# Kernel optimization log

Measured on AMD Instinct MI355X. Metric: run time of the kernel, lower is better.

## Reference

```python
import jax, jax.numpy as jnp
import numpy as np
from functools import partial

MIN_PERSISTENCE = 0.0
BIG = jnp.float32(1e30)


def pairwise_dist(points):
    # points: [n, d] -> [n, n] Euclidean distances (Vietoris-Rips filtration values on edges)
    sq = jnp.sum(points * points, axis=-1)
    d2 = sq[:, None] + sq[None, :] - 2.0 * (points @ points.T)
    return jnp.sqrt(jnp.clip(d2, 0.0))


def h0_persistence(points):
    """0-dim persistent homology of the Vietoris-Rips filtration.

    H0 bars: every point is born at filtration 0; components merge at MST edge
    lengths (single-linkage). Deaths = the n-1 MST edge weights, in the order
    Prim's algorithm adds them (the boundary-matrix column reduction for dim 0
    yields exactly these pairs). One essential class (infinite bar) is dropped.
    """
    n = points.shape[0]
    dist = pairwise_dist(points)  # [n, n]

    in_tree = jnp.zeros((n,), dtype=bool).at[0].set(True)
    mind = dist[0]  # min distance from each node to the current tree

    def step(carry, _):
        mind, in_tree = carry
        masked = jnp.where(in_tree, BIG, mind)
        j = jnp.argmin(masked)          # next vertex merged into the tree
        death = masked[j]               # filtration value at which its component dies
        in_tree = in_tree.at[j].set(True)
        mind = jnp.minimum(mind, dist[j])
        return (mind, in_tree), death

    (_, _), deaths = jax.lax.scan(step, (mind, in_tree), None, length=n - 1)

    births = jnp.zeros_like(deaths)
    diagram = jnp.stack([births, deaths], axis=-1)  # [n-1, 2]
    # min_persistence threshold: zero out bars with persistence below threshold
    keep = (deaths - births) >= MIN_PERSISTENCE
    return jnp.where(keep[:, None], diagram, 0.0)


def setup_inputs() -> dict:
    key = jax.random.key(0)
    x = jax.random.normal(key, (8192, 64), dtype=jnp.float32)
    return {"x": x}


def reference(x):
    # PersistentHomologyLayer.forward with edge_index=None -> point-cloud VR persistence.
    return h0_persistence(x)
```

## Files before the change

kernel.cpp:

```cpp
#include <hip/hip_runtime.h>
#include <math.h>

#define N 8192
#define DIM 64
#define CAP_E 2000000

typedef unsigned long long u64;
typedef unsigned int u32;
typedef unsigned short u16;

__global__ void zero_out_kernel(float* __restrict__ out, int n) {
    int i = blockIdx.x * blockDim.x + threadIdx.x;
    if (i < n) out[i] = 0.0f;
}

__global__ __launch_bounds__(256) void norms_kernel(const float* __restrict__ x,
                                                    float* __restrict__ norms) {
    int i = blockIdx.x * blockDim.x + threadIdx.x;
    const float* row = x + (size_t)i * DIM;
    float acc = 0.f;
    #pragma unroll
    for (int k = 0; k < DIM; k++) { float v = row[k]; acc = __builtin_fmaf(v, v, acc); }
    norms[i] = acc;
}

__device__ inline void stage_tiles(const float* __restrict__ x, int bi, int bj, int t,
                                   float (*As)[64], float (*Bs)[64]) {
    int r = t >> 2, c0 = (t & 3) * 16;
    const float4* pa = (const float4*)(x + (size_t)(bi * 64 + r) * DIM + c0);
    const float4* pb = (const float4*)(x + (size_t)(bj * 64 + r) * DIM + c0);
    #pragma unroll
    for (int q = 0; q < 4; q++) {
        float4 a = pa[q], b = pb[q];
        int c = c0 + q * 4;
        As[c + 0][r] = a.x; As[c + 1][r] = a.y; As[c + 2][r] = a.z; As[c + 3][r] = a.w;
        Bs[c + 0][r] = b.x; Bs[c + 1][r] = b.y; Bs[c + 2][r] = b.z; Bs[c + 3][r] = b.w;
    }
}

__device__ inline void tile_d2(const float (*As)[64], const float (*Bs)[64],
                               const float ni[4], const float nj[4],
                               int tx, int ty, u32 d2b[4][4]) {
    float acc[4][4] = {};
    #pragma unroll 4
    for (int k = 0; k < 64; k++) {
        float av[4], bv[4];
        #pragma unroll
        for (int r = 0; r < 4; r++) av[r] = As[k][ty * 4 + r];
        #pragma unroll
        for (int c = 0; c < 4; c++) bv[c] = Bs[k][tx * 4 + c];
        #pragma unroll
        for (int r = 0; r < 4; r++)
            #pragma unroll
            for (int c = 0; c < 4; c++)
                acc[r][c] = __builtin_fmaf(av[r], bv[c], acc[r][c]);
    }
    #pragma unroll
    for (int r = 0; r < 4; r++)
        #pragma unroll
        for (int c = 0; c < 4; c++) {
            float d2 = __builtin_fmaf(-2.0f, acc[r][c], ni[r] + nj[c]);
            d2 = d2 < 0.f ? 0.f : d2;
            d2b[r][c] = __float_as_uint(d2);
        }
}

__global__ void init_kernel(u64* bestR, u64* bestC, u16* comp16, u32* deg, u32* ctr) {
    int i = blockIdx.x * blockDim.x + threadIdx.x;
    if (i < 8192) { bestR[i] = ~0ull; bestC[i] = ~0ull; comp16[i] = (u16)i; deg[i] = 0; }
    if (i < 8) ctr[i] = 0;
}

__global__ __launch_bounds__(256) void scan_fused(const float* __restrict__ x,
                                                  const float* __restrict__ norms,
                                                  const u16* __restrict__ comp16,
                                                  u64* __restrict__ bestR,
                                                  const u32* __restrict__ ctr) {
    if (ctr[1]) return;
    int bi = blockIdx.y, bj = blockIdx.x;
    if (bj < bi) return;
    __shared__ float As[64][64], Bs[64][64];
    __shared__ u16 rc[64], cc[64];
    __shared__ u64 rowBest[64], colBest[64];
    int t = threadIdx.x;
    stage_tiles(x, bi, bj, t, As, Bs);
    if (t < 64) {
        rc[t] = comp16[bi * 64 + t];
        cc[t] = comp16[bj * 64 + t];
        rowBest[t] = ~0ull; colBest[t] = ~0ull;
    }
    __syncthreads();
    int tx = t & 15, ty = t >> 4;
    float ni[4], nj[4];
    #pragma unroll
    for (int r = 0; r < 4; r++) ni[r] = norms[bi * 64 + ty * 4 + r];
    #pragma unroll
    for (int c = 0; c < 4; c++) nj[c] = norms[bj * 64 + tx * 4 + c];
    u32 d2b[4][4];
    tile_d2(As, Bs, ni, nj, tx, ty, d2b);

    #pragma unroll
    for (int r = 0; r < 4; r++) {
        u16 rcv = rc[ty * 4 + r];
        int gi = bi * 64 + ty * 4 + r;
        u64 best = ~0ull;
        #pragma unroll
        for (int c = 0; c < 4; c++) {
            if (cc[tx * 4 + c] != rcv) {
                int gj = bj * 64 + tx * 4 + c;
                u32 lo = gi < gj ? (u32)gi : (u32)gj;
                u32 hi = gi < gj ? (u32)gj : (u32)gi;
                u64 key = ((u64)d2b[r][c] << 26) | ((u64)lo << 13) | hi;
                if (key < best) best = key;
            }
        }
        if (best != ~0ull) atomicMin(&rowBest[ty * 4 + r], best);
    }
    #pragma unroll
    for (int c = 0; c < 4; c++) {
        u16 ccv = cc[tx * 4 + c];
        int gj = bj * 64 + tx * 4 + c;
        u64 best = ~0ull;
        #pragma unroll
        for (int r = 0; r < 4; r++) {
            if (rc[ty * 4 + r] != ccv) {
                int gi = bi * 64 + ty * 4 + r;
                u32 lo = gi < gj ? (u32)gi : (u32)gj;
                u32 hi = gi < gj ? (u32)gj : (u32)gi;
                u64 key = ((u64)d2b[r][c] << 26) | ((u64)lo << 13) | hi;
                if (key < best) best = key;
            }
        }
        if (best != ~0ull) atomicMin(&colBest[tx * 4 + c], best);
    }
    __syncthreads();
    if (t < 64) {
        if (rowBest[t] != ~0ull) atomicMin(&bestR[bi * 64 + t], rowBest[t]);
        if (colBest[t] != ~0ull) atomicMin(&bestR[bj * 64 + t], colBest[t]);
    }
}

__global__ void fold_kernel(u64* bestR, u64* bestC, const u16* comp16, const u32* ctr) {
    if (ctr[1]) return;
    int i = blockIdx.x * blockDim.x + threadIdx.x;
    if (i < 8192) {
        u64 k = bestR[i];
        if (k != ~0ull) { atomicMin(&bestC[comp16[i]], k); bestR[i] = ~0ull; }
    }
}

__global__ __launch_bounds__(1024) void merge_kernel(u16* comp16, u64* bestC,
                                                     u64* mstKeys, u32* ctr) {
    __shared__ u16 ping[8192], pong[8192];
    __shared__ unsigned char act[8192];
    __shared__ u32 cnt_s;
    if (ctr[1]) return;
    int t = threadIdx.x;
    if (t == 0) cnt_s = 0;
    for (int c = t; c < 8192; c += 1024) {
        u64 key = bestC[c];
        u16 par = (u16)c;
        if (key != ~0ull) {
            u32 a = (u32)(key >> 13) & 8191u, b = (u32)key & 8191u;
            u16 ca = comp16[a];
            u16 cv = (ca == (u16)c) ? comp16[b] : ca;
            u64 k2 = bestC[cv];
            bool mutual = false;
            if (k2 != ~0ull) {
                u32 a2 = (u32)(k2 >> 13) & 8191u, b2 = (u32)k2 & 8191u;
                u16 ca2 = comp16[a2];
                u16 cv2 = (ca2 == cv) ? comp16[b2] : ca2;
                mutual = (cv2 == (u16)c);
            }
            par = cv;
            if (mutual && (u32)c < (u32)cv) par = (u16)c;
            bool add = (!mutual) || ((u32)c < (u32)cv);
            if (add) {
                u32 idx = atomicAdd(&ctr[0], 1u);
                if (idx < 8192u) mstKeys[idx] = key;
            }
        }
        ping[c] = par;
        act[c] = 0;
    }
    __syncthreads();
    for (int c = t; c < 8192; c += 1024) bestC[c] = ~0ull;
    __syncthreads();
    for (int it = 0; it < 13; it++) {
        for (int c = t; c < 8192; c += 1024) pong[c] = ping[ping[c]];
        __syncthreads();
        for (int c = t; c < 8192; c += 1024) ping[c] = pong[c];
        __syncthreads();
    }
    for (int v = t; v < 8192; v += 1024) {
        u16 nc = ping[comp16[v]];
        comp16[v] = nc;
        act[nc] = 1;
    }
    __syncthreads();
    u32 local = 0;
    for (int c = t; c < 8192; c += 1024) local += act[c];
    atomicAdd(&cnt_s, local);
    __syncthreads();
    if (t == 0 && cnt_s == 1) ctr[1] = 1;
}

__global__ __launch_bounds__(1024) void sort_kernel(const u64* __restrict__ mstKeys,
                                                    u32* __restrict__ sortedWB,
                                                    const u32* __restrict__ ctr) {
    __shared__ u64 keys[8192];
    int t = threadIdx.x;
    u32 m = ctr[0]; if (m > 8191u) m = 8191u;
    for (int i = t; i < 8192; i += 1024) keys[i] = (i < (int)m) ? mstKeys[i] : ~0ull;
    __syncthreads();
    for (u32 k = 2; k <= 8192; k <<= 1)
        for (u32 j = k >> 1; j > 0; j >>= 1) {
            for (int i = t; i < 8192; i += 1024) {
                u32 ixj = (u32)i ^ j;
                if (ixj > (u32)i) {
                    u64 a = keys[i], b = keys[ixj];
                    bool up = ((i & k) == 0);
                    if ((a > b) == up) { keys[i] = b; keys[ixj] = a; }
                }
            }
            __syncthreads();
        }
    for (int i = t; i < 8192; i += 1024)
        sortedWB[i] = (i < 8191) ? (u32)(keys[i] >> 26) : 0xFFFFFFFFu;
}

__global__ __launch_bounds__(256) void collect_kernel(const float* __restrict__ x,
                                                      const float* __restrict__ norms,
                                                      const u32* __restrict__ sortedWB,
                                                      u64* __restrict__ edges,
                                                      u32* __restrict__ ctr) {
    __shared__ float As[64][64], Bs[64][64];
    __shared__ u32 sw[8191];
    int bi = blockIdx.y, bj = blockIdx.x;
    if (bj < bi) return;
    int t = threadIdx.x;
    stage_tiles(x, bi, bj, t, As, Bs);
    for (int i = t; i < 8191; i += 256) sw[i] = sortedWB[i];
    __syncthreads();
    u32 wmin = sw[0], wmax = sw[8190];
    int tx = t & 15, ty = t >> 4;
    float ni[4], nj[4];
    #pragma unroll
    for (int r = 0; r < 4; r++) ni[r] = norms[bi * 64 + ty * 4 + r];
    #pragma unroll
    for (int c = 0; c < 4; c++) nj[c] = norms[bj * 64 + tx * 4 + c];
    u32 d2b[4][4];
    tile_d2(As, Bs, ni, nj, tx, ty, d2b);

    #pragma unroll
    for (int r = 0; r < 4; r++) {
        int gi = bi * 64 + ty * 4 + r;
        #pragma unroll
        for (int c = 0; c < 4; c++) {
            int gj = bj * 64 + tx * 4 + c;
            if (gj <= gi) continue;
            u32 wb = d2b[r][c];
            if (wb < wmin || wb > wmax) continue;
            int lo = 0, hi = 8190;
            while (lo < hi) { int mid = (lo + hi) >> 1; if (sw[mid] < wb) lo = mid + 1; else hi = mid; }
            if (sw[lo] == wb) {
                u32 idx = atomicAdd(&ctr[3], 1u);
                if (idx < CAP_E)
                    edges[idx] = ((u64)(u32)lo << 26) | ((u64)(u32)gi << 13) | (u32)gj;
                else
                    atomicOr(&ctr[2], 16u);
            }
        }
    }
}

__global__ void degcnt_kernel(const u64* __restrict__ edges, u32* __restrict__ deg,
                              const u32* __restrict__ ctr) {
    u32 m = ctr[3]; if (m > CAP_E) m = CAP_E;
    for (u32 idx = blockIdx.x * 256u + threadIdx.x; idx < m; idx += gridDim.x * 256u) {
        u64 e = edges[idx];
        atomicAdd(&deg[(u32)(e >> 13) & 8191u], 1u);
        atomicAdd(&deg[(u32)e & 8191u], 1u);
    }
}

__global__ __launch_bounds__(1024) void offs_kernel(const u32* __restrict__ deg,
                                                    u32* __restrict__ offs,
                                                    u32* __restrict__ cur) {
    __shared__ u32 partial[1024];
    int t = threadIdx.x;
    u32 loc[8], s = 0;
    #pragma unroll
    for (int e = 0; e < 8; e++) { loc[e] = deg[t * 8 + e]; s += loc[e]; }
    partial[t] = s;
    __syncthreads();
    for (int d = 1; d < 1024; d <<= 1) {
        u32 v = (t >= d) ? partial[t - d] : 0;
        __syncthreads();
        partial[t] += v;
        __syncthreads();
    }
    u32 run = t ? partial[t - 1] : 0;
    #pragma unroll
    for (int e = 0; e < 8; e++) { offs[t * 8 + e] = run; cur[t * 8 + e] = run; run += loc[e]; }
    if (t == 1023) offs[8192] = run;
}

__global__ void fill_kernel(const u64* __restrict__ edges, u32* __restrict__ cur,
                            u32* __restrict__ adj, const u32* __restrict__ ctr) {
    u32 m = ctr[3]; if (m > CAP_E) m = CAP_E;
    for (u32 idx = blockIdx.x * 256u + threadIdx.x; idx < m; idx += gridDim.x * 256u) {
        u64 e = edges[idx];
        u32 rk = (u32)(e >> 26) & 8191u;
        u32 i = (u32)(e >> 13) & 8191u, j = (u32)e & 8191u;
        u32 p1 = atomicAdd(&cur[i], 1u); adj[p1] = (rk << 13) | j;
        u32 p2 = atomicAdd(&cur[j], 1u); adj[p2] = (rk << 13) | i;
    }
}

__device__ __forceinline__ u32 dpp_min_u32(u32 x) {
    u32 y;
    y = (u32)__builtin_amdgcn_update_dpp((int)0xFFFFFFFF, (int)x, 0x111, 0xf, 0xf, false); x = y < x ? y : x;
    y = (u32)__builtin_amdgcn_update_dpp((int)0xFFFFFFFF, (int)x, 0x112, 0xf, 0xf, false); x = y < x ? y : x;
    y = (u32)__builtin_amdgcn_update_dpp((int)0xFFFFFFFF, (int)x, 0x114, 0xf, 0xf, false); x = y < x ? y : x;
    y = (u32)__builtin_amdgcn_update_dpp((int)0xFFFFFFFF, (int)x, 0x118, 0xf, 0xf, false); x = y < x ? y : x;
    y = (u32)__builtin_amdgcn_update_dpp((int)0xFFFFFFFF, (int)x, 0x142, 0xa, 0xf, false); x = y < x ? y : x;
    y = (u32)__builtin_amdgcn_update_dpp((int)0xFFFFFFFF, (int)x, 0x143, 0xc, 0xf, false); x = y < x ? y : x;
    return x;
}

__global__ __launch_bounds__(256) void gprim_kernel(const u32* __restrict__ offs,
                                                    const u32* __restrict__ adjG,
                                                    u32* __restrict__ seqv,
                                                    u32* __restrict__ ctr) {
    __shared__ u16 sMind[8192];
    __shared__ u32 sOffs[8193];
    __shared__ u32 sAdj[16384];
    const int t = threadIdx.x;
    for (int i = t; i < 8193; i += 256) sOffs[i] = offs[i];
    { u32* p = (u32*)sMind; for (int i = t; i < 4096; i += 256) p[i] = 0x3FFF3FFFu; }
    u32 m = ctr[3]; if (m > CAP_E) m = CAP_E;
    u32 tot = 2u * m;
    const bool useLds = (tot <= 16384u);
    if (useLds) {
        const uint4* a4 = (const uint4*)adjG; uint4* s4 = (uint4*)sAdj;
        u32 tot4 = (tot + 3u) >> 2;
        for (u32 i = (u32)t; i < tot4; i += 256u) s4[i] = a4[i];
    }
    __syncthreads();
    if (t >= 64) return;
    const int lane = t;
    if (lane == 0) sMind[0] = 0xFFFFu;
    u64 ins0 = (lane == 0) ? 1ull : 0ull, ins1 = 0ull;
    u32 cmin = 0xFFFFFFFFu;
    u32 v = 0u, Lv = 0u;

#define PROC(e, pred) do { \
        u32 _far = (e) & 8191u, _rk = (e) >> 13; \
        if ((pred) && (((_far ^ (u32)lane) & 63u) == 0u)) { \
            u32 _slot = _far >> 6; \
            u64 _w = (_slot & 64u) ? ins1 : ins0; \
            if (((_w >> (_slot & 63u)) & 1ull) == 0ull) { \
                u32 _k = (_rk << 13) | _far; \
                if (_k < patch) patch = _k; \
                u32 _loc = ((u32)lane << 7) + _slot; \
                u16 _old = sMind[_loc]; \
                if ((u16)_rk < _old) sMind[_loc] = (u16)_rk; \
            } \
        } \
    } while (0)

    for (int step = 0; step < N - 1; ++step) {
        u32 rowPair = ((const u32*)sMind)[(Lv << 6) + (u32)lane];
        u32 o0 = sOffs[v], o1 = sOffs[v + 1];
        u32 dg = o1 - o0;
        u32 iL = (o1 > o0) ? (o1 - 1u) : o0;
        u32 patch = 0xFFFFFFFFu;
        {
            u32 i1 = (o0 + 1u > iL) ? iL : o0 + 1u;
            u32 i2 = (o0 + 2u > iL) ? iL : o0 + 2u;
            u32 i3 = (o0 + 3u > iL) ? iL : o0 + 3u;
            u32 e0, e1, e2, e3;
            if (useLds) { e0 = sAdj[o0]; e1 = sAdj[i1]; e2 = sAdj[i2]; e3 = sAdj[i3]; }
            else        { e0 = adjG[o0]; e1 = adjG[i1]; e2 = adjG[i2]; e3 = adjG[i3]; }
            PROC(e0, dg > 0u); PROC(e1, dg > 1u); PROC(e2, dg > 2u); PROC(e3, dg > 3u);
            for (u32 q = 4u; q < dg; ++q) {
                u32 e = useLds ? sAdj[o0 + q] : adjG[o0 + q];
                PROC(e, true);
            }
        }
        cmin = patch < cmin ? patch : cmin;
        u32 m0 = rowPair & 0xFFFFu, m1 = rowPair >> 16;
        u32 s0 = ((u32)lane << 1), s1 = s0 + 1u;
        u32 vslot = v >> 6;
        u32 k0 = (m0 < 0x3FFFu && s0 != vslot) ? ((m0 << 13) | (s0 << 6) | Lv) : 0xFFFFFFFFu;
        u32 k1 = (m1 < 0x3FFFu && s1 != vslot) ? ((m1 << 13) | (s1 << 6) | Lv) : 0xFFFFFFFFu;
        u32 rowMin = k0 < k1 ? k0 : k1;
        u32 R = dpp_min_u32(rowMin);
        u32 xc = ((u32)lane == Lv) ? patch : cmin;
        u32 C = dpp_min_u32(xc);
        u32 Rs = (u32)__builtin_amdgcn_readlane((int)R, 63);
        u32 Cs = (u32)__builtin_amdgcn_readlane((int)C, 63);
        u32 g = Rs < Cs ? Rs : Cs;
        if ((u32)lane == Lv) cmin = Rs < patch ? Rs : patch;
        if (g >= (0x3FFFu << 13)) { if (lane == 0) atomicOr(&ctr[2], 2u); break; }
        if (lane == 0) seqv[step] = g;
        v = g & 8191u; Lv = v & 63u;
        if ((u32)lane == Lv) {
            u32 nslot = v >> 6;
            if (nslot < 64u) ins0 |= 1ull << nslot; else ins1 |= 1ull << (nslot - 64u);
            sMind[(Lv << 7) + nslot] = 0xFFFFu;
        }
    }
#undef PROC
}

__global__ void gather_kernel(const u32* __restrict__ seqv,
                              const u32* __restrict__ sortedWB,
                              float* __restrict__ out) {
    int s = blockIdx.x * blockDim.x + threadIdx.x;
    if (s < N - 1) {
        u32 p = seqv[s];
        u32 rk = p >> 13;
        out[2 * s + 1] = sqrtf(__uint_as_float(sortedWB[rk]));
    }
}

extern "C" void kernel_launch(void* const* d_in, const int* in_sizes, int n_in,
                              void* d_out, int out_size, void* d_ws, size_t ws_size,
                              hipStream_t stream) {
    const float* x = (const float*)d_in[0];
    float* out = (float*)d_out;

    char* ws = (char*)d_ws;
    size_t o = 0;
    u64* bestR    = (u64*)(ws + o); o += 8192 * 8;
    u64* bestC    = (u64*)(ws + o); o += 8192 * 8;
    u64* mstKeys  = (u64*)(ws + o); o += 8192 * 8;
    u64* edges    = (u64*)(ws + o); o += (size_t)CAP_E * 8;
    float* norms  = (float*)(ws + o); o += 8192 * 4;
    u32* sortedWB = (u32*)(ws + o); o += 8192 * 4;
    u32* deg      = (u32*)(ws + o); o += 8192 * 4;
    u32* offs     = (u32*)(ws + o); o += 8200 * 4;
    u32* cur      = (u32*)(ws + o); o += 8192 * 4;
    u32* seqv     = (u32*)(ws + o); o += 8192 * 4;
    u32* adj      = (u32*)(ws + o); o += (size_t)CAP_E * 2 * 4;
    u16* comp16   = (u16*)(ws + o); o += 8192 * 2;
    u32* ctr      = (u32*)(ws + o); o += 256;

    zero_out_kernel<<<(out_size + 255) / 256, 256, 0, stream>>>(out, out_size);
    norms_kernel<<<32, 256, 0, stream>>>(x, norms);
    init_kernel<<<32, 256, 0, stream>>>(bestR, bestC, comp16, deg, ctr);

    for (int r = 0; r < 13; r++) {
        scan_fused<<<dim3(128, 128), 256, 0, stream>>>(x, norms, comp16, bestR, ctr);
        fold_kernel<<<32, 256, 0, stream>>>(bestR, bestC, comp16, ctr);
        merge_kernel<<<1, 1024, 0, stream>>>(comp16, bestC, mstKeys, ctr);
    }

    sort_kernel<<<1, 1024, 0, stream>>>(mstKeys, sortedWB, ctr);
    collect_kernel<<<dim3(128, 128), 256, 0, stream>>>(x, norms, sortedWB, edges, ctr);
    degcnt_kernel<<<512, 256, 0, stream>>>(edges, deg, ctr);
    offs_kernel<<<1, 1024, 0, stream>>>(deg, offs, cur);
    fill_kernel<<<512, 256, 0, stream>>>(edges, cur, adj, ctr);
    gprim_kernel<<<1, 256, 0, stream>>>(offs, adj, seqv, ctr);
    gather_kernel<<<32, 256, 0, stream>>>(seqv, sortedWB, out);
}
```

Baseline: 7.181 ms.

## Pack per-vertex adjacency into LDS uint4 slots and pad GEMM tiles

Adds a kernel that packs the first three or four neighbours of each vertex into a 16-byte slot, plus an overflow record for high-degree vertices. The single-block Prim kernel then does one LDS load per step instead of offset lookups and clamped indexing, and falls back to global memory only for vertices with more than four neighbours. It also pads the shared tile arrays to 65 columns to avoid LDS bank conflicts in the distance tiles. The overflow path now always reads global memory even when the full adjacency would have fit in LDS, and the extra kernel adds a launch.

```diff
diff --git a/kernel.cpp b/kernel.cpp
--- a/kernel.cpp
+++ b/kernel.cpp
@@ -25,7 +25,7 @@
 }
 
 __device__ inline void stage_tiles(const float* __restrict__ x, int bi, int bj, int t,
-                                   float (*As)[64], float (*Bs)[64]) {
+                                   float (*As)[65], float (*Bs)[65]) {
     int r = t >> 2, c0 = (t & 3) * 16;
     const float4* pa = (const float4*)(x + (size_t)(bi * 64 + r) * DIM + c0);
     const float4* pb = (const float4*)(x + (size_t)(bj * 64 + r) * DIM + c0);
@@ -38,7 +38,7 @@
     }
 }
 
-__device__ inline void tile_d2(const float (*As)[64], const float (*Bs)[64],
+__device__ inline void tile_d2(const float (*As)[65], const float (*Bs)[65],
                                const float ni[4], const float nj[4],
                                int tx, int ty, u32 d2b[4][4]) {
     float acc[4][4] = {};
@@ -79,7 +79,7 @@
     if (ctr[1]) return;
     int bi = blockIdx.y, bj = blockIdx.x;
     if (bj < bi) return;
-    __shared__ float As[64][64], Bs[64][64];
+    __shared__ float As[64][65], Bs[64][65];
     __shared__ u16 rc[64], cc[64];
     __shared__ u64 rowBest[64], colBest[64];
     int t = threadIdx.x;
@@ -234,7 +234,7 @@
                                                       const u32* __restrict__ sortedWB,
                                                       u64* __restrict__ edges,
                                                       u32* __restrict__ ctr) {
-    __shared__ float As[64][64], Bs[64][64];
+    __shared__ float As[64][65], Bs[64][65];
     __shared__ u32 sw[8191];
     int bi = blockIdx.y, bj = blockIdx.x;
     if (bj < bi) return;
@@ -318,6 +318,21 @@
     }
 }
 
+__global__ __launch_bounds__(256) void adj4_kernel(const u32* __restrict__ offs,
+                                                   const u32* __restrict__ adjG,
+                                                   uint4* __restrict__ adj4,
+                                                   u64* __restrict__ ovf) {
+    int v = blockIdx.x * 256 + threadIdx.x;
+    if (v >= N) return;
+    u32 o0 = offs[v], o1 = offs[v + 1], dg = o1 - o0;
+    u32 e[4] = {0xFFFFFFFFu, 0xFFFFFFFFu, 0xFFFFFFFFu, 0xFFFFFFFFu};
+    u32 nin = dg <= 4u ? dg : 3u;
+    for (u32 q = 0; q < nin; q++) e[q] = adjG[o0 + q];
+    if (dg > 4u) e[3] = 0xFFFFFFFEu;
+    adj4[v] = make_uint4(e[0], e[1], e[2], e[3]);
+    ovf[v] = ((u64)dg << 32) | o0;
+}
+
 __device__ __forceinline__ u32 dpp_min_u32(u32 x) {
     u32 y;
     y = (u32)__builtin_amdgcn_update_dpp((int)0xFFFFFFFF, (int)x, 0x111, 0xf, 0xf, false); x = y < x ? y : x;
@@ -329,24 +344,16 @@
     return x;
 }
 
-__global__ __launch_bounds__(256) void gprim_kernel(const u32* __restrict__ offs,
+__global__ __launch_bounds__(256) void gprim_kernel(const uint4* __restrict__ adj4,
+                                                    const u64* __restrict__ ovf,
                                                     const u32* __restrict__ adjG,
                                                     u32* __restrict__ seqv,
                                                     u32* __restrict__ ctr) {
+    __shared__ uint4 sAdj4[8192];
     __shared__ u16 sMind[8192];
-    __shared__ u32 sOffs[8193];
-    __shared__ u32 sAdj[16384];
     const int t = threadIdx.x;
-    for (int i = t; i < 8193; i += 256) sOffs[i] = offs[i];
+    for (int i = t; i < 8192; i += 256) sAdj4[i] = adj4[i];
     { u32* p = (u32*)sMind; for (int i = t; i < 4096; i += 256) p[i] = 0x3FFF3FFFu; }
-    u32 m = ctr[3]; if (m > CAP_E) m = CAP_E;
-    u32 tot = 2u * m;
-    const bool useLds = (tot <= 16384u);
-    if (useLds) {
-        const uint4* a4 = (const uint4*)adjG; uint4* s4 = (uint4*)sAdj;
-        u32 tot4 = (tot + 3u) >> 2;
-        for (u32 i = (u32)t; i < tot4; i += 256u) s4[i] = a4[i];
-    }
     __syncthreads();
     if (t >= 64) return;
     const int lane = t;
@@ -355,14 +362,14 @@
     u32 cmin = 0xFFFFFFFFu;
     u32 v = 0u, Lv = 0u;
 
-#define PROC(e, pred) do { \
-        u32 _far = (e) & 8191u, _rk = (e) >> 13; \
-        if ((pred) && (((_far ^ (u32)lane) & 63u) == 0u)) { \
+#define PROC(e) do { \
+        u32 _e = (e); \
+        if (_e < 0x04000000u && (((_e ^ (u32)lane) & 63u) == 0u)) { \
+            u32 _far = _e & 8191u, _rk = _e >> 13; \
             u32 _slot = _far >> 6; \
             u64 _w = (_slot & 64u) ? ins1 : ins0; \
             if (((_w >> (_slot & 63u)) & 1ull) == 0ull) { \
-                u32 _k = (_rk << 13) | _far; \
-                if (_k < patch) patch = _k; \
+                if (_e < patch) patch = _e; \
                 u32 _loc = ((u32)lane << 7) + _slot; \
                 u16 _old = sMind[_loc]; \
                 if ((u16)_rk < _old) sMind[_loc] = (u16)_rk; \
@@ -372,22 +379,21 @@
 
     for (int step = 0; step < N - 1; ++step) {
         u32 rowPair = ((const u32*)sMind)[(Lv << 6) + (u32)lane];
-        u32 o0 = sOffs[v], o1 = sOffs[v + 1];
-        u32 dg = o1 - o0;
-        u32 iL = (o1 > o0) ? (o1 - 1u) : o0;
+        uint4 A = sAdj4[v];
         u32 patch = 0xFFFFFFFFu;
-        {
-            u32 i1 = (o0 + 1u > iL) ? iL : o0 + 1u;
-            u32 i2 = (o0 + 2u > iL) ? iL : o0 + 2u;
-            u32 i3 = (o0 + 3u > iL) ? iL : o0 + 3u;
-            u32 e0, e1, e2, e3;
-            if (useLds) { e0 = sAdj[o0]; e1 = sAdj[i1]; e2 = sAdj[i2]; e3 = sAdj[i3]; }
-            else        { e0 = adjG[o0]; e1 = adjG[i1]; e2 = adjG[i2]; e3 = adjG[i3]; }
-            PROC(e0, dg > 0u); PROC(e1, dg > 1u); PROC(e2, dg > 2u); PROC(e3, dg > 3u);
-            for (u32 q = 4u; q < dg; ++q) {
-                u32 e = useLds ? sAdj[o0 + q] : adjG[o0 + q];
-                PROC(e, true);
-            }
+        PROC(A.x); PROC(A.y); PROC(A.z);
+        if (A.w == 0xFFFFFFFEu) {
+            u64 od = ovf[v];
+            u32 o0 = (u32)od, dgv = (u32)(od >> 32);
+            u32 q = 3;
+            for (; q + 4 <= dgv; q += 4) {
+                u32 e0 = adjG[o0 + q], e1 = adjG[o0 + q + 1];
+                u32 e2 = adjG[o0 + q + 2], e3 = adjG[o0 + q + 3];
+                PROC(e0); PROC(e1); PROC(e2); PROC(e3);
+            }
+            for (; q < dgv; q++) { u32 e = adjG[o0 + q]; PROC(e); }
+        } else {
+            PROC(A.w);
         }
         cmin = patch < cmin ? patch : cmin;
         u32 m0 = rowPair & 0xFFFFu, m1 = rowPair >> 16;
@@ -445,6 +451,8 @@
     u32* cur      = (u32*)(ws + o); o += 8192 * 4;
     u32* seqv     = (u32*)(ws + o); o += 8192 * 4;
     u32* adj      = (u32*)(ws + o); o += (size_t)CAP_E * 2 * 4;
+    uint4* adj4   = (uint4*)(ws + o); o += 8192 * 16;
+    u64* ovf      = (u64*)(ws + o); o += 8192 * 8;
     u16* comp16   = (u16*)(ws + o); o += 8192 * 2;
     u32* ctr      = (u32*)(ws + o); o += 256;
 
@@ -463,6 +471,7 @@
     degcnt_kernel<<<512, 256, 0, stream>>>(edges, deg, ctr);
     offs_kernel<<<1, 1024, 0, stream>>>(deg, offs, cur);
     fill_kernel<<<512, 256, 0, stream>>>(edges, cur, adj, ctr);
-    gprim_kernel<<<1, 256, 0, stream>>>(offs, adj, seqv, ctr);
+    adj4_kernel<<<32, 256, 0, stream>>>(offs, adj, adj4, ovf);
+    gprim_kernel<<<1, 256, 0, stream>>>(adj4, ovf, adj, seqv, ctr);
     gather_kernel<<<32, 256, 0, stream>>>(seqv, sortedWB, out);
 }
```

After: 6.256 ms. -12.9%, faster.
